# Optimization experiments

Hardware: AMD Instinct MI355X
Metric: run time of the kernel (lower is better)

## Reference

```python
import jax, jax.numpy as jnp
import numpy as np


def _avgpool(x, k):
    # x: [B, C, H, W] -> [B, C, H//k, W//k] via non-overlapping mean pooling
    B, C, H, W = x.shape
    return x.reshape(B, C, H // k, k, W // k, k).mean(axis=(3, 5))


def _multiscale_tokens(x):
    # concat flattened pooled maps along token dim: [B, C, sum_k (H/k)*(W/k)]
    B, C, H, W = x.shape
    parts = [_avgpool(x, k).reshape(B, C, -1) for k in (16, 8, 4, 2)]
    return jnp.concatenate(parts, axis=2)


def setup_inputs() -> dict:
    key = jax.random.key(0)
    x = jax.random.normal(key, (16, 256, 128, 128), dtype=jnp.float32)
    gamma = jnp.zeros((1,), dtype=jnp.float32)
    return {"x": x, "gamma": gamma}


def reference(x, gamma):
    B, C, H, W = x.shape
    # q and k pooling are identical in the original module (recomputed redundantly)
    tokens = _multiscale_tokens(x)                      # [B, C, T]
    energy = jnp.einsum('bct,bdt->bcd', tokens, tokens)  # [B, C, C]
    energy_new = jnp.max(energy, axis=-1, keepdims=True) - energy
    attention = jax.nn.softmax(energy_new, axis=-1)      # [B, C, C]
    proj_value = x.reshape(B, C, H * W)                  # [B, C, HW]
    out = jnp.einsum('bcd,bdn->bcn', attention, proj_value).reshape(B, C, H, W)
    return gamma * out + x
```

## Files before the change

### kernel.cpp

```cpp
#include <hip/hip_runtime.h>
#include <hip/hip_bf16.h>

#define B_  16
#define C_  256
#define W_  128
#define HW_ 16384
#define T_  5440
#define NSPLIT 10

typedef __bf16 bf16;
typedef __bf16 bf16x2 __attribute__((ext_vector_type(2)));
typedef __bf16 bf16x4 __attribute__((ext_vector_type(4)));
typedef __bf16 bf16x8 __attribute__((ext_vector_type(8)));
typedef float  f32x4  __attribute__((ext_vector_type(4)));

__device__ __forceinline__ void gload_lds16(const void* g, void* l) {
    __builtin_amdgcn_global_load_lds(
        (const __attribute__((address_space(1))) void*)g,
        (__attribute__((address_space(3))) void*)l, 16, 0, 0);
}

__device__ __forceinline__ int bs_addr(int n, int q4) {
    return (n & 3) * 2048 + q4 * 512 + (((n >> 2) ^ (q4 << 1)) & 31) * 16;
}

__global__ __launch_bounds__(256) void pool_kernel(const float* __restrict__ x,
                                                   bf16* __restrict__ tokens) {
    __shared__ float s2[64 * 64];
    __shared__ float s4[32 * 32];
    __shared__ float s8[16 * 16];
    const int blk = blockIdx.x;
    const float* plane = x + ((size_t)blk << 14);
    bf16* tok = tokens + (size_t)blk * T_;
    const int tid = threadIdx.x;

    for (int it = 0; it < 8; ++it) {
        int task = it * 256 + tid;
        int i  = task >> 5;
        int jp = task & 31;
        const float4 r0 = *(const float4*)(plane + (2 * i) * W_ + 4 * jp);
        const float4 r1 = *(const float4*)(plane + (2 * i + 1) * W_ + 4 * jp);
        float p0 = (r0.x + r0.y + r1.x + r1.y) * 0.25f;
        float p1 = (r0.z + r0.w + r1.z + r1.w) * 0.25f;
        s2[i * 64 + 2 * jp]     = p0;
        s2[i * 64 + 2 * jp + 1] = p1;
        bf16x2 wv; wv.x = (bf16)p0; wv.y = (bf16)p1;
        *(bf16x2*)(tok + 1344 + i * 64 + 2 * jp) = wv;
    }
    __syncthreads();
    for (int it = 0; it < 4; ++it) {
        int task = it * 256 + tid;
        int i = task >> 5, j = task & 31;
        float v = 0.25f * (s2[(2 * i) * 64 + 2 * j] + s2[(2 * i) * 64 + 2 * j + 1] +
                           s2[(2 * i + 1) * 64 + 2 * j] + s2[(2 * i + 1) * 64 + 2 * j + 1]);
        s4[i * 32 + j] = v;
        tok[320 + i * 32 + j] = (bf16)v;
    }
    __syncthreads();
    {
        int i = tid >> 4, j = tid & 15;
        float v = 0.25f * (s4[(2 * i) * 32 + 2 * j] + s4[(2 * i) * 32 + 2 * j + 1] +
                           s4[(2 * i + 1) * 32 + 2 * j] + s4[(2 * i + 1) * 32 + 2 * j + 1]);
        s8[i * 16 + j] = v;
        tok[64 + tid] = (bf16)v;
    }
    __syncthreads();
    if (tid < 64) {
        int i = tid >> 3, j = tid & 7;
        float v = 0.25f * (s8[(2 * i) * 16 + 2 * j] + s8[(2 * i) * 16 + 2 * j + 1] +
                           s8[(2 * i + 1) * 16 + 2 * j] + s8[(2 * i + 1) * 16 + 2 * j + 1]);
        tok[tid] = (bf16)v;
    }
}

__global__ __launch_bounds__(256) void energy_kernel(const bf16* __restrict__ tokens,
                                                     float* __restrict__ part) {
    __shared__ bf16 As[128 * 40];
    __shared__ bf16 Bs[128 * 40];
    const int blk  = blockIdx.x;
    const int s    = blk >> 6;
    const int rem  = blk & 63;
    const int b    = rem >> 2;
    const int tile = rem & 3;
    const int cm0  = (tile >> 1) << 7;
    const int cn0  = (tile & 1) << 7;
    const int kbase = s * (T_ / NSPLIT);
    const int tid  = threadIdx.x;
    const int lane = tid & 63;
    const int w    = tid >> 6;
    const int wm = (w >> 1) * 64, wn = (w & 1) * 64;
    const int lm = lane & 15;
    const int q8 = (lane >> 4) * 8;
    f32x4 acc[4][4] = {};
    for (int ki = 0; ki < (T_ / NSPLIT) / 32; ++ki) {
        const int k0 = kbase + ki * 32;
        __syncthreads();
        for (int it = 0; it < 2; ++it) {
            int slot = it * 256 + tid;
            int r   = slot >> 2;
            int c8  = (slot & 3) * 8;
            *(int4*)(As + r * 40 + c8) = *(const int4*)(tokens + (size_t)(b * C_ + cm0 + r) * T_ + k0 + c8);
            *(int4*)(Bs + r * 40 + c8) = *(const int4*)(tokens + (size_t)(b * C_ + cn0 + r) * T_ + k0 + c8);
        }
        __syncthreads();
        bf16x8 af[4], bfr[4];
        for (int mi = 0; mi < 4; ++mi)
            af[mi] = *(const bf16x8*)(As + (wm + mi * 16 + lm) * 40 + q8);
        for (int ni = 0; ni < 4; ++ni)
            bfr[ni] = *(const bf16x8*)(Bs + (wn + ni * 16 + lm) * 40 + q8);
        for (int mi = 0; mi < 4; ++mi)
            for (int ni = 0; ni < 4; ++ni)
                acc[mi][ni] = __builtin_amdgcn_mfma_f32_16x16x32_bf16(af[mi], bfr[ni], acc[mi][ni], 0, 0, 0);
    }
    float* P = part + ((size_t)(s * 4096 + b * C_) << 8);
    const int row0 = (lane >> 4) * 4;
    for (int mi = 0; mi < 4; ++mi)
        for (int ni = 0; ni < 4; ++ni) {
            f32x4 v = acc[mi][ni];
            int row = cm0 + wm + mi * 16 + row0;
            int col = cn0 + wn + ni * 16 + lm;
            for (int e = 0; e < 4; ++e)
                P[((size_t)(row + e) << 8) + col] = v[e];
        }
}

__global__ __launch_bounds__(256) void softmax_kernel(const float* __restrict__ part,
                                                      bf16* __restrict__ att) {
    const int row  = blockIdx.x * 4 + (threadIdx.x >> 6);
    const int lane = threadIdx.x & 63;
    float4 e = {0.f, 0.f, 0.f, 0.f};
    for (int s = 0; s < NSPLIT; ++s) {
        const float4 p = *(const float4*)(part + ((size_t)(s * 4096 + row) << 8) + lane * 4);
        e.x += p.x; e.y += p.y; e.z += p.z; e.w += p.w;
    }
    float mn = fminf(fminf(e.x, e.y), fminf(e.z, e.w));
    for (int off = 32; off > 0; off >>= 1) mn = fminf(mn, __shfl_xor(mn, off));
    float p0 = __expf(mn - e.x), p1 = __expf(mn - e.y);
    float p2 = __expf(mn - e.z), p3 = __expf(mn - e.w);
    float s = p0 + p1 + p2 + p3;
    for (int off = 32; off > 0; off >>= 1) s += __shfl_xor(s, off);
    float inv = 1.0f / s;
    bf16x4 o;
    o.x = (bf16)(p0 * inv); o.y = (bf16)(p1 * inv);
    o.z = (bf16)(p2 * inv); o.w = (bf16)(p3 * inv);
    *(bf16x4*)(att + ((size_t)row << 8) + lane * 4) = o;
}

__global__ __launch_bounds__(256, 2) void out_kernel(const bf16* __restrict__ att,
                                                     const float* __restrict__ x,
                                                     const float* __restrict__ gamma,
                                                     float* __restrict__ out) {
    __shared__ __align__(16) char smem[33792];
    bf16* As  = (bf16*)smem;
    char* BsB = smem + 16384;
    const int b  = blockIdx.x >> 7;
    const int n0 = (blockIdx.x & 127) << 7;
    const int tid  = threadIdx.x;
    const int lane = tid & 63;
    const int w    = tid >> 6;
    const int wm   = w * 64;
    const int lm = lane & 15;
    const int q4 = lane >> 4;
    const int q8 = q4 * 8;
    const float g = gamma[0];
    const bf16* attb = att + ((size_t)b << 16);
    const int cg = tid & 31;
    const int kq = tid >> 5;
    const float* xsrc = x + ((size_t)b << 22) + ((size_t)(kq * 4) << 14) + n0 + cg * 4;

    f32x4 acc[4][8] = {};
    f32x4 vj[4];
    #pragma unroll
    for (int j = 0; j < 4; ++j) vj[j] = *(const f32x4*)(xsrc + ((size_t)j << 14));

    for (int kk = 0; kk < 8; ++kk) {
        const int k0 = kk * 32;
        __syncthreads();
        #pragma unroll
        for (int it = 0; it < 4; ++it) {
            int slot = it * 256 + w * 64 + lane;
            int r  = slot >> 2;
            int c8 = (slot & 3) * 8;
            gload_lds16(attb + ((size_t)r << 8) + k0 + c8,
                        As + (size_t)(it * 256 + w * 64) * 8);
        }
        {
            const int gq = kq >> 1;
            const int h  = (kq & 1) * 8;
            #pragma unroll
            for (int e = 0; e < 4; ++e) {
                bf16x4 wv;
                wv.x = (bf16)vj[0][e]; wv.y = (bf16)vj[1][e];
                wv.z = (bf16)vj[2][e]; wv.w = (bf16)vj[3][e];
                *(bf16x4*)(BsB + bs_addr(cg * 4 + e, gq) + h) = wv;
            }
        }
        __syncthreads();
        if (kk < 7) {
            const float* xs2 = xsrc + ((size_t)(kk + 1) << 19);
            #pragma unroll
            for (int j = 0; j < 4; ++j) vj[j] = *(const f32x4*)(xs2 + ((size_t)j << 14));
        }
        bf16x8 af[4];
        #pragma unroll
        for (int mi = 0; mi < 4; ++mi)
            af[mi] = *(const bf16x8*)(As + (wm + mi * 16 + lm) * 32 + q8);
        #pragma unroll
        for (int ni = 0; ni < 8; ++ni) {
            bf16x8 bfr = *(const bf16x8*)(BsB + bs_addr(ni * 16 + lm, q4));
            #pragma unroll
            for (int mi = 0; mi < 4; ++mi)
                acc[mi][ni] = __builtin_amdgcn_mfma_f32_16x16x32_bf16(af[mi], bfr, acc[mi][ni], 0, 0, 0);
        }
    }
    float* buf = (float*)(smem + w * 8448);
    __syncthreads();
    for (int mi = 0; mi < 4; ++mi) {
        #pragma unroll
        for (int ni = 0; ni < 8; ++ni) {
            f32x4 v = acc[mi][ni];
            int c = ni * 16 + lm;
            buf[(q4 * 4 + 0) * 132 + c] = v[0];
            buf[(q4 * 4 + 1) * 132 + c] = v[1];
            buf[(q4 * 4 + 2) * 132 + c] = v[2];
            buf[(q4 * 4 + 3) * 132 + c] = v[3];
        }
        __syncthreads();
        #pragma unroll
        for (int t = 0; t < 8; ++t) {
            int idx = t * 64 + lane;
            int r  = idx >> 5;
            int c4 = (idx & 31) * 4;
            f32x4 pv = *(const f32x4*)(buf + r * 132 + c4);
            int c = wm + mi * 16 + r;
            size_t gi = ((size_t)b << 22) + ((size_t)c << 14) + n0 + c4;
            float4 xv = *(const float4*)(x + gi);
            float4 o;
            o.x = g * pv[0] + xv.x;
            o.y = g * pv[1] + xv.y;
            o.z = g * pv[2] + xv.z;
            o.w = g * pv[3] + xv.w;
            *(float4*)(out + gi) = o;
        }
        __syncthreads();
    }
}

__global__ __launch_bounds__(256) void fallback_copy(const float* __restrict__ x,
                                                     const float* __restrict__ gamma,
                                                     float* __restrict__ out, size_t n) {
    size_t i = (size_t)blockIdx.x * 256 + threadIdx.x;
    size_t stride = (size_t)gridDim.x * 256;
    float g = gamma[0];
    for (; i < n; i += stride) out[i] = x[i] + g * 0.0f;
}

extern "C" void kernel_launch(void* const* d_in, const int* in_sizes, int n_in,
                              void* d_out, int out_size, void* d_ws, size_t ws_size,
                              hipStream_t stream) {
    const float* x     = (const float*)d_in[0];
    const float* gamma = (const float*)d_in[1];
    float* out = (float*)d_out;

    const size_t ATT_BYTES = (size_t)B_ * C_ * C_ * 2;
    if (ws_size < ATT_BYTES) {
        size_t n = (size_t)B_ * C_ * HW_;
        fallback_copy<<<2048, 256, 0, stream>>>(x, gamma, out, n);
        return;
    }
    bf16*  tokens = (bf16*)d_out;
    float* part   = (float*)((char*)d_out + ((size_t)64 << 20));
    bf16*  att    = (bf16*)d_ws;

    pool_kernel<<<dim3(B_ * C_), dim3(256), 0, stream>>>(x, tokens);
    energy_kernel<<<dim3(NSPLIT * B_ * 4), dim3(256), 0, stream>>>(tokens, part);
    softmax_kernel<<<dim3(B_ * C_ / 4), dim3(256), 0, stream>>>(part, att);
    out_kernel<<<dim3(B_ * 128), dim3(256), 0, stream>>>(att, x, gamma, out);
}
```

Baseline: 586.5 us.

## Exploit energy symmetry, double-buffer loads, and reuse staged x tile in output kernel

The energy GEMM now computes only three of the four 128x128 tiles per batch, mirroring the off-diagonal tile into its transpose, and double-buffers token tiles through direct global-to-LDS loads. The output kernel switches to 512-thread blocks with 64-column tiles. It stages the fp32 x slice in LDS so the residual add reuses it instead of re-reading x from global memory, double-buffers the attention and value tiles, and writes the output with nontemporal stores. In exchange the kernel uses much more LDS per block (about 104 KB), which may limit occupancy, and the energy blocks carry an uneven workload.

```diff
diff --git a/kernel.cpp b/kernel.cpp
--- a/kernel.cpp
+++ b/kernel.cpp
@@ -20,8 +20,8 @@
         (__attribute__((address_space(3))) void*)l, 16, 0, 0);
 }
 
-__device__ __forceinline__ int bs_addr(int n, int q4) {
-    return (n & 3) * 2048 + q4 * 512 + (((n >> 2) ^ (q4 << 1)) & 31) * 16;
+__device__ __forceinline__ int bs64(int n, int q) {
+    return (n & 3) * 1024 + q * 256 + (((n >> 2) ^ (q << 1)) & 15) * 16;
 }
 
 __global__ __launch_bounds__(256) void pool_kernel(const float* __restrict__ x,
@@ -73,17 +73,17 @@
     }
 }
 
-__global__ __launch_bounds__(256) void energy_kernel(const bf16* __restrict__ tokens,
-                                                     float* __restrict__ part) {
-    __shared__ bf16 As[128 * 40];
-    __shared__ bf16 Bs[128 * 40];
+__global__ __launch_bounds__(256, 2) void energy_kernel(const bf16* __restrict__ tokens,
+                                                        float* __restrict__ part) {
+    __shared__ __align__(16) char smem[32768];
     const int blk  = blockIdx.x;
-    const int s    = blk >> 6;
-    const int rem  = blk & 63;
-    const int b    = rem >> 2;
-    const int tile = rem & 3;
-    const int cm0  = (tile >> 1) << 7;
-    const int cn0  = (tile & 1) << 7;
+    const int s    = blk / 48;
+    const int rem  = blk - s * 48;
+    const int b    = rem / 3;
+    const int tile = rem - b * 3;
+    const int cm0  = (tile == 2) ? 128 : 0;
+    const int cn0  = (tile == 0) ? 0 : 128;
+    const bool offdiag = (tile == 1);
     const int kbase = s * (T_ / NSPLIT);
     const int tid  = threadIdx.x;
     const int lane = tid & 63;
@@ -91,27 +91,52 @@
     const int wm = (w >> 1) * 64, wn = (w & 1) * 64;
     const int lm = lane & 15;
     const int q8 = (lane >> 4) * 8;
+    const bf16* tokb = tokens + (size_t)b * C_ * T_;
+
+    #define E_STAGE(ki, d) do {                                                   \
+        const int k0_ = kbase + (ki) * 32;                                        \
+        _Pragma("unroll")                                                         \
+        for (int it = 0; it < 2; ++it) {                                          \
+            int slot = it * 256 + tid;                                            \
+            int r  = slot >> 2;                                                   \
+            int c8 = (slot & 3) * 8;                                              \
+            gload_lds16(tokb + (size_t)(cm0 + r) * T_ + k0_ + c8,                 \
+                        smem + (size_t)(d) * 8192 + (size_t)(it * 256 + w * 64) * 16); \
+        }                                                                         \
+        if (offdiag) {                                                            \
+            _Pragma("unroll")                                                     \
+            for (int it = 0; it < 2; ++it) {                                      \
+                int slot = it * 256 + tid;                                        \
+                int r  = slot >> 2;                                               \
+                int c8 = (slot & 3) * 8;                                          \
+                gload_lds16(tokb + (size_t)(cn0 + r) * T_ + k0_ + c8,             \
+                            smem + 16384 + (size_t)(d) * 8192 + (size_t)(it * 256 + w * 64) * 16); \
+            }                                                                     \
+        }                                                                         \
+    } while (0)
+
     f32x4 acc[4][4] = {};
-    for (int ki = 0; ki < (T_ / NSPLIT) / 32; ++ki) {
-        const int k0 = kbase + ki * 32;
-        __syncthreads();
-        for (int it = 0; it < 2; ++it) {
-            int slot = it * 256 + tid;
-            int r   = slot >> 2;
-            int c8  = (slot & 3) * 8;
-            *(int4*)(As + r * 40 + c8) = *(const int4*)(tokens + (size_t)(b * C_ + cm0 + r) * T_ + k0 + c8);
-            *(int4*)(Bs + r * 40 + c8) = *(const int4*)(tokens + (size_t)(b * C_ + cn0 + r) * T_ + k0 + c8);
-        }
-        __syncthreads();
+    E_STAGE(0, 0);
+    __syncthreads();
+    for (int ki = 0; ki < 17; ++ki) {
+        if (ki < 16) E_STAGE(ki + 1, (ki + 1) & 1);
+        const bf16* Af = (const bf16*)(smem + (ki & 1) * 8192);
+        const bf16* Bf = offdiag ? (const bf16*)(smem + 16384 + (ki & 1) * 8192) : Af;
         bf16x8 af[4], bfr[4];
+        #pragma unroll
         for (int mi = 0; mi < 4; ++mi)
-            af[mi] = *(const bf16x8*)(As + (wm + mi * 16 + lm) * 40 + q8);
+            af[mi] = *(const bf16x8*)(Af + (wm + mi * 16 + lm) * 32 + q8);
+        #pragma unroll
         for (int ni = 0; ni < 4; ++ni)
-            bfr[ni] = *(const bf16x8*)(Bs + (wn + ni * 16 + lm) * 40 + q8);
+            bfr[ni] = *(const bf16x8*)(Bf + (wn + ni * 16 + lm) * 32 + q8);
+        #pragma unroll
         for (int mi = 0; mi < 4; ++mi)
+            #pragma unroll
             for (int ni = 0; ni < 4; ++ni)
                 acc[mi][ni] = __builtin_amdgcn_mfma_f32_16x16x32_bf16(af[mi], bfr[ni], acc[mi][ni], 0, 0, 0);
-    }
+        __syncthreads();
+    }
+    #undef E_STAGE
     float* P = part + ((size_t)(s * 4096 + b * C_) << 8);
     const int row0 = (lane >> 4) * 4;
     for (int mi = 0; mi < 4; ++mi)
@@ -119,8 +144,11 @@
             f32x4 v = acc[mi][ni];
             int row = cm0 + wm + mi * 16 + row0;
             int col = cn0 + wn + ni * 16 + lm;
+            #pragma unroll
             for (int e = 0; e < 4; ++e)
                 P[((size_t)(row + e) << 8) + col] = v[e];
+            if (offdiag)
+                *(f32x4*)(P + ((size_t)col << 8) + row) = v;
         }
 }
 
@@ -146,103 +174,122 @@
     *(bf16x4*)(att + ((size_t)row << 8) + lane * 4) = o;
 }
 
-__global__ __launch_bounds__(256, 2) void out_kernel(const bf16* __restrict__ att,
+__global__ __launch_bounds__(512, 2) void out_kernel(const bf16* __restrict__ att,
                                                      const float* __restrict__ x,
                                                      const float* __restrict__ gamma,
                                                      float* __restrict__ out) {
-    __shared__ __align__(16) char smem[33792];
-    bf16* As  = (bf16*)smem;
-    char* BsB = smem + 16384;
-    const int b  = blockIdx.x >> 7;
-    const int n0 = (blockIdx.x & 127) << 7;
+    __shared__ __align__(16) char smem[106496];
+    float* Vf = (float*)smem;
+    const int b  = blockIdx.x >> 8;
+    const int n0 = (blockIdx.x & 255) << 6;
     const int tid  = threadIdx.x;
     const int lane = tid & 63;
     const int w    = tid >> 6;
-    const int wm   = w * 64;
+    const int wm   = w * 32;
     const int lm = lane & 15;
     const int q4 = lane >> 4;
     const int q8 = q4 * 8;
     const float g = gamma[0];
-    const bf16* attb = att + ((size_t)b << 16);
-    const int cg = tid & 31;
-    const int kq = tid >> 5;
-    const float* xsrc = x + ((size_t)b << 22) + ((size_t)(kq * 4) << 14) + n0 + cg * 4;
-
-    f32x4 acc[4][8] = {};
-    f32x4 vj[4];
-    #pragma unroll
-    for (int j = 0; j < 4; ++j) vj[j] = *(const f32x4*)(xsrc + ((size_t)j << 14));
+    const bf16*  attb = att + ((size_t)b << 16);
+    const float* xb   = x + ((size_t)b << 22);
+    const int gn = tid & 15;
+    const int kp = tid >> 4;
+    const bool vthread = (tid < 256);
+
+    #define A_STAGE(kk, d) do {                                                   \
+        const int k0_ = (kk) * 32;                                                \
+        _Pragma("unroll")                                                         \
+        for (int it = 0; it < 2; ++it) {                                          \
+            int slot = it * 512 + tid;                                            \
+            int r  = slot >> 2;                                                   \
+            int c8 = (slot & 3) * 8;                                              \
+            gload_lds16(attb + ((size_t)r << 8) + k0_ + c8,                       \
+                        smem + 65536 + (size_t)(d) * 16384 + (size_t)(it * 512 + w * 64) * 16); \
+        }                                                                         \
+    } while (0)
+
+    f32x4 acc[2][4] = {};
+    f32x4 vj0, vj1;
+
+    if (vthread) {
+        vj0 = *(const f32x4*)(xb + ((size_t)(2 * kp) << 14) + n0 + gn * 4);
+        vj1 = *(const f32x4*)(xb + ((size_t)(2 * kp + 1) << 14) + n0 + gn * 4);
+        *(f32x4*)(Vf + (2 * kp) * 64 + gn * 4)     = vj0;
+        *(f32x4*)(Vf + (2 * kp + 1) * 64 + gn * 4) = vj1;
+        char* Bs0 = smem + 98304;
+        #pragma unroll
+        for (int e = 0; e < 4; ++e) {
+            bf16x2 wv; wv.x = (bf16)vj0[e]; wv.y = (bf16)vj1[e];
+            *(bf16x2*)(Bs0 + bs64(gn * 4 + e, kp >> 2) + 4 * (kp & 3)) = wv;
+        }
+    }
+    A_STAGE(0, 0);
+    __syncthreads();
 
     for (int kk = 0; kk < 8; ++kk) {
-        const int k0 = kk * 32;
-        __syncthreads();
-        #pragma unroll
-        for (int it = 0; it < 4; ++it) {
-            int slot = it * 256 + w * 64 + lane;
-            int r  = slot >> 2;
-            int c8 = (slot & 3) * 8;
-            gload_lds16(attb + ((size_t)r << 8) + k0 + c8,
-                        As + (size_t)(it * 256 + w * 64) * 8);
-        }
-        {
-            const int gq = kq >> 1;
-            const int h  = (kq & 1) * 8;
+        if (kk < 7) {
+            if (vthread) {
+                const float* xs = xb + ((size_t)((kk + 1) * 32 + 2 * kp) << 14) + n0 + gn * 4;
+                vj0 = *(const f32x4*)(xs);
+                vj1 = *(const f32x4*)(xs + HW_);
+            }
+            A_STAGE(kk + 1, (kk + 1) & 1);
+        }
+        const bf16* Af  = (const bf16*)(smem + 65536 + (kk & 1) * 16384);
+        const char* BsR = smem + 98304 + (kk & 1) * 4096;
+        bf16x8 af[2];
+        #pragma unroll
+        for (int mi = 0; mi < 2; ++mi)
+            af[mi] = *(const bf16x8*)(Af + (wm + mi * 16 + lm) * 32 + q8);
+        #pragma unroll
+        for (int ni = 0; ni < 4; ++ni) {
+            bf16x8 bb = *(const bf16x8*)(BsR + bs64(ni * 16 + lm, q4));
+            #pragma unroll
+            for (int mi = 0; mi < 2; ++mi)
+                acc[mi][ni] = __builtin_amdgcn_mfma_f32_16x16x32_bf16(af[mi], bb, acc[mi][ni], 0, 0, 0);
+        }
+        if (kk < 7 && vthread) {
+            const int c0 = (kk + 1) * 32 + 2 * kp;
+            *(f32x4*)(Vf + (c0)     * 64 + gn * 4) = vj0;
+            *(f32x4*)(Vf + (c0 + 1) * 64 + gn * 4) = vj1;
+            char* BsW = smem + 98304 + ((kk + 1) & 1) * 4096;
             #pragma unroll
             for (int e = 0; e < 4; ++e) {
-                bf16x4 wv;
-                wv.x = (bf16)vj[0][e]; wv.y = (bf16)vj[1][e];
-                wv.z = (bf16)vj[2][e]; wv.w = (bf16)vj[3][e];
-                *(bf16x4*)(BsB + bs_addr(cg * 4 + e, gq) + h) = wv;
+                bf16x2 wv; wv.x = (bf16)vj0[e]; wv.y = (bf16)vj1[e];
+                *(bf16x2*)(BsW + bs64(gn * 4 + e, kp >> 2) + 4 * (kp & 3)) = wv;
             }
         }
         __syncthreads();
-        if (kk < 7) {
-            const float* xs2 = xsrc + ((size_t)(kk + 1) << 19);
-            #pragma unroll
-            for (int j = 0; j < 4; ++j) vj[j] = *(const f32x4*)(xs2 + ((size_t)j << 14));
-        }
-        bf16x8 af[4];
-        #pragma unroll
-        for (int mi = 0; mi < 4; ++mi)
-            af[mi] = *(const bf16x8*)(As + (wm + mi * 16 + lm) * 32 + q8);
-        #pragma unroll
-        for (int ni = 0; ni < 8; ++ni) {
-            bf16x8 bfr = *(const bf16x8*)(BsB + bs_addr(ni * 16 + lm, q4));
-            #pragma unroll
-            for (int mi = 0; mi < 4; ++mi)
-                acc[mi][ni] = __builtin_amdgcn_mfma_f32_16x16x32_bf16(af[mi], bfr, acc[mi][ni], 0, 0, 0);
-        }
-    }
-    float* buf = (float*)(smem + w * 8448);
-    __syncthreads();
-    for (int mi = 0; mi < 4; ++mi) {
-        #pragma unroll
-        for (int ni = 0; ni < 8; ++ni) {
+    }
+    #undef A_STAGE
+
+    float* buf = (float*)(smem + 65536) + w * 1024;
+    for (int mi = 0; mi < 2; ++mi) {
+        #pragma unroll
+        for (int ni = 0; ni < 4; ++ni) {
             f32x4 v = acc[mi][ni];
             int c = ni * 16 + lm;
-            buf[(q4 * 4 + 0) * 132 + c] = v[0];
-            buf[(q4 * 4 + 1) * 132 + c] = v[1];
-            buf[(q4 * 4 + 2) * 132 + c] = v[2];
-            buf[(q4 * 4 + 3) * 132 + c] = v[3];
-        }
-        __syncthreads();
-        #pragma unroll
-        for (int t = 0; t < 8; ++t) {
-            int idx = t * 64 + lane;
-            int r  = idx >> 5;
-            int c4 = (idx & 31) * 4;
-            f32x4 pv = *(const f32x4*)(buf + r * 132 + c4);
+            buf[(q4 * 4 + 0) * 64 + c] = v[0];
+            buf[(q4 * 4 + 1) * 64 + c] = v[1];
+            buf[(q4 * 4 + 2) * 64 + c] = v[2];
+            buf[(q4 * 4 + 3) * 64 + c] = v[3];
+        }
+        #pragma unroll
+        for (int it = 0; it < 4; ++it) {
+            int idx = it * 64 + lane;
+            int r  = idx >> 4;
+            int c4 = (idx & 15) * 4;
+            f32x4 pv = *(const f32x4*)(buf + r * 64 + c4);
             int c = wm + mi * 16 + r;
+            f32x4 xv = *(const f32x4*)(Vf + c * 64 + c4);
+            f32x4 o;
+            o[0] = g * pv[0] + xv[0];
+            o[1] = g * pv[1] + xv[1];
+            o[2] = g * pv[2] + xv[2];
+            o[3] = g * pv[3] + xv[3];
             size_t gi = ((size_t)b << 22) + ((size_t)c << 14) + n0 + c4;
-            float4 xv = *(const float4*)(x + gi);
-            float4 o;
-            o.x = g * pv[0] + xv.x;
-            o.y = g * pv[1] + xv.y;
-            o.z = g * pv[2] + xv.z;
-            o.w = g * pv[3] + xv.w;
-            *(float4*)(out + gi) = o;
-        }
-        __syncthreads();
+            __builtin_nontemporal_store(o, (f32x4*)(out + gi));
+        }
     }
 }
 
@@ -273,7 +320,7 @@
     bf16*  att    = (bf16*)d_ws;
 
     pool_kernel<<<dim3(B_ * C_), dim3(256), 0, stream>>>(x, tokens);
-    energy_kernel<<<dim3(NSPLIT * B_ * 4), dim3(256), 0, stream>>>(tokens, part);
+    energy_kernel<<<dim3(NSPLIT * B_ * 3), dim3(256), 0, stream>>>(tokens, part);
     softmax_kernel<<<dim3(B_ * C_ / 4), dim3(256), 0, stream>>>(part, att);
-    out_kernel<<<dim3(B_ * 128), dim3(256), 0, stream>>>(att, x, gamma, out);
-}
+    out_kernel<<<dim3(B_ * 256), dim3(512), 0, stream>>>(att, x, gamma, out);
+}
```

Result: no change. 579.9 us (-1.1%).
